# Performance work log

Measured on AMD Instinct MI355X. Metric: run time of the kernel, lower is better.

Reference implementation:

```python
import jax, jax.numpy as jnp
import numpy as np

N_NODES = 50000
N_EDGES = 800000
IN_C, HID_C, OUT_C = 256, 256, 64


def _glorot(key, shape):
    fan_in, fan_out = shape[1], shape[0]
    lim = float(np.sqrt(6.0 / (fan_in + fan_out)))
    return jax.random.uniform(key, shape, jnp.float32, -lim, lim)


def setup_inputs() -> dict:
    key = jax.random.key(0)
    ks = jax.random.split(key, 8)
    x = jax.random.normal(ks[0], (N_NODES, IN_C), jnp.float32)
    edge_index = jax.random.randint(ks[1], (2, N_EDGES), 0, N_NODES, jnp.int64)
    # layer 1: SAGEConv(IN_C -> HID_C): lin_l (agg neighbors, has bias), lin_r (root, no bias)
    W_l1 = _glorot(ks[2], (HID_C, IN_C))
    b1 = jnp.zeros((HID_C,), jnp.float32)
    W_r1 = _glorot(ks[3], (HID_C, IN_C))
    # layer 2: SAGEConv(HID_C -> OUT_C)
    W_l2 = _glorot(ks[4], (OUT_C, HID_C))
    b2 = jnp.zeros((OUT_C,), jnp.float32)
    W_r2 = _glorot(ks[5], (OUT_C, HID_C))
    return {"x": x, "W_l1": W_l1, "b1": b1, "W_r1": W_r1,
            "W_l2": W_l2, "b2": b2, "W_r2": W_r2, "edge_index": edge_index}


def _sage_conv(x, src, dst, W_l, b, W_r, n_nodes):
    # mean aggregation of source-node features into destination nodes
    msg = x[src]                                               # [E, C]
    agg = jax.ops.segment_sum(msg, dst, num_segments=n_nodes)  # [N, C]
    deg = jax.ops.segment_sum(jnp.ones((src.shape[0],), x.dtype), dst,
                              num_segments=n_nodes)            # [N]
    agg = agg / jnp.maximum(deg, 1.0)[:, None]
    # out = lin_l(agg) + lin_r(x); bias only on lin_l (PyG SAGEConv default)
    return agg @ W_l.T + b + x @ W_r.T


def reference(x, W_l1, b1, W_r1, W_l2, b2, W_r2, edge_index):
    src, dst = edge_index[0], edge_index[1]
    n = x.shape[0]
    h = _sage_conv(x, src, dst, W_l1, b1, W_r1, n)
    h = jax.nn.relu(h)  # dropout is identity in eval mode
    out = _sage_conv(h, src, dst, W_l2, b2, W_r2, n)
    return out
```

## Files before the change

### kernel.cpp

```cpp
#include <hip/hip_runtime.h>

#define IN_C 256
#define HID_C 256
#define OUT_C 64

#define NBK 64
#define NPAD 50176
#define N2 (NPAD / 2)
#define NCH (NPAD / 256)

typedef __attribute__((ext_vector_type(8))) short bf16x8;
typedef __attribute__((ext_vector_type(4))) float f32x4;
typedef __attribute__((ext_vector_type(2))) float f32x2;
typedef __attribute__((ext_vector_type(8))) unsigned short ushortx8;
typedef __attribute__((ext_vector_type(4))) unsigned int u32x4;
typedef __attribute__((ext_vector_type(2))) unsigned int u32x2;

__device__ inline float b2f(unsigned short u) {
    union { unsigned int u; float f; } v; v.u = ((unsigned int)u) << 16; return v.f;
}
__device__ inline unsigned short f2b(float f) {
    union { float f; unsigned int u; } v; v.f = f;
    unsigned int u = v.u;
    unsigned int r = (u + 0x7fffu + ((u >> 16) & 1u)) >> 16;
    return (unsigned short)r;
}

__device__ __forceinline__ unsigned char f2fp8(float v) {
    int pk = __builtin_amdgcn_cvt_pk_fp8_f32(v, v, 0, false);
    return (unsigned char)(pk & 0xff);
}
__device__ __forceinline__ void fp8acc4(unsigned int w, float& a0, float& a1, float& a2, float& a3) {
    f32x2 lo = __builtin_amdgcn_cvt_pk_f32_fp8((int)w, false);
    f32x2 hi = __builtin_amdgcn_cvt_pk_f32_fp8((int)w, true);
    a0 += lo.x; a1 += lo.y; a2 += hi.x; a3 += hi.y;
}

__device__ __forceinline__ void gl2lds16(const ushort* g, ushort* l) {
    __builtin_amdgcn_global_load_lds((const __attribute__((address_space(1))) void*)g,
                                     (__attribute__((address_space(3))) void*)l, 16, 0, 0);
}

__device__ __forceinline__ void conv8(const float* __restrict__ src, ushort* __restrict__ dst, int u) {
    const float4* p = (const float4*)(src + (size_t)u * 8);
    float4 a = p[0], b = p[1];
    ushort4 o0 = make_ushort4(f2b(a.x), f2b(a.y), f2b(a.z), f2b(a.w));
    ushort4 o1 = make_ushort4(f2b(b.x), f2b(b.y), f2b(b.z), f2b(b.w));
    ((ushort4*)(dst + (size_t)u * 8))[0] = o0;
    ((ushort4*)(dst + (size_t)u * 8))[1] = o1;
}


__global__ __launch_bounds__(1024) void k_front(const int* __restrict__ dst, int E, int EPB,
                                                ushort* __restrict__ rank,
                                                unsigned int* __restrict__ cnt32,
                                                int* __restrict__ chunkpart,
                                                const float* __restrict__ x, ushort* __restrict__ xb,
                                                int xUnits,
                                                const float* __restrict__ Wl1, const float* __restrict__ Wr1,
                                                const float* __restrict__ Wl2, const float* __restrict__ Wr2,
                                                ushort* __restrict__ Wc1, ushort* __restrict__ Wc2) {
    const int bid = blockIdx.x;
    const int t = threadIdx.x;

    if (bid < NBK) {
        __shared__ unsigned int h[N2];
        for (int i = t; i < N2; i += 1024) h[i] = 0;
        __syncthreads();

        const int e0 = bid * EPB;
        const int e1 = min(e0 + EPB, E);
        for (int e = e0 + t; e < e1; e += 1024) {
            int d = dst[e];
            int sh = (d & 1) << 4;
            unsigned int old = atomicAdd(&h[d >> 1], 1u << sh);
            rank[e] = (ushort)((old >> sh) & 0xffffu);
        }
        __syncthreads();

        unsigned int* outp = cnt32 + (size_t)bid * N2;
        for (int i = t; i < N2; i += 1024) outp[i] = h[i];

        if (t < NCH) {
            int c = t;
            int sum = 0;
#pragma unroll 8
            for (int j = 0; j < 128; ++j) {
                unsigned int v = h[c * 128 + ((j + c) & 127)];
                sum += (int)(v & 0xffffu) + (int)(v >> 16);
            }
            chunkpart[c * NBK + bid] = sum;
        }
        return;
    }

    const int ct = (bid - NBK) * 1024 + t;
    const int cn = 256 * 1024;
    for (int i = ct; i < 20480; i += cn) {
        if (i < 8192)       conv8(Wl1, Wc1,         i);
        else if (i < 16384) conv8(Wr1, Wc1 + 65536, i - 8192);
        else if (i < 18432) conv8(Wl2, Wc2,         i - 16384);
        else                conv8(Wr2, Wc2 + 16384, i - 18432);
    }
    for (int u = ct; u < xUnits; u += cn) conv8(x, xb, u);
}


__global__ __launch_bounds__(256) void k_scan(const unsigned int* __restrict__ cnt32,
                                              const int* __restrict__ chunkpart, int N,
                                              int* __restrict__ row_start,
                                              ushort* __restrict__ off16) {
    __shared__ int s[256];
    const int bid = blockIdx.x;
    const int t = threadIdx.x;

    int pre = 0;
    const int limit = bid * NBK;
    for (int i = t; i < limit; i += 256) pre += chunkpart[i];
    s[t] = pre;
    __syncthreads();
    for (int o = 128; o > 0; o >>= 1) {
        if (t < o) s[t] += s[t + o];
        __syncthreads();
    }
    const int chunk_off = s[0];
    __syncthreads();

    const int i = bid * 256 + t;
    const ushort* cnt16 = (const ushort*)cnt32;
    int run = 0;
#pragma unroll 8
    for (int b = 0; b < NBK; ++b) {
        ushort cv = cnt16[(size_t)b * NPAD + i];
        off16[(size_t)b * NPAD + i] = (ushort)run;
        run += cv;
    }
    int deg = run;

    s[t] = deg;
    __syncthreads();
    for (int o = 1; o < 256; o <<= 1) {
        int xx = (t >= o) ? s[t - o] : 0;
        __syncthreads();
        s[t] += xx;
        __syncthreads();
    }
    if (i < N) row_start[i + 1] = s[t] + chunk_off;
    if (i == 0) row_start[0] = 0;
}


__global__ __launch_bounds__(256) void k_gemm_mfma(const ushort* __restrict__ A,
                                                   const ushort* __restrict__ W,
                                                   unsigned char* __restrict__ Cp,
                                                   ushort* __restrict__ Cr,
                                                   int N, int K, int PC, int nby, int nwg,
                                                   int nScat,
                                                   const int* __restrict__ src, const int* __restrict__ dst,
                                                   const ushort* __restrict__ rank,
                                                   const int* __restrict__ row_start,
                                                   const ushort* __restrict__ off16,
                                                   int E, int EPB, int* __restrict__ eidx) {
    if (blockIdx.x < (unsigned)nScat) {
        int base = blockIdx.x * 256 + threadIdx.x;
        int stride = nScat * 256;
        for (int e = base; e < E; e += stride) {
            int d = dst[e];
            int b = e / EPB;
            eidx[row_start[d] + (int)off16[(size_t)b * NPAD + d] + (int)rank[e]] = src[e];
        }
        return;
    }

    __shared__ ushort As[2][128 * 64];
    __shared__ ushort Bs[2][128 * 64];

    const int orig = blockIdx.x - nScat;
    const int q = nwg >> 3, r = nwg & 7;
    const int xcd = orig & 7;
    const int base = (xcd < r) ? xcd * (q + 1) : r * (q + 1) + (xcd - r) * q;
    const int wgid = base + (orig >> 3);
    const int bx = wgid / nby, by = wgid % nby;

    const int wid  = threadIdx.x >> 6;
    const int lane = threadIdx.x & 63;
    const int wr = wid >> 1, wc = wid & 1;
    const int bm = bx * 128;
    const int bn = by * 128;
    const int lr = lane & 15;
    const int lk = lane >> 4;
    const int srow   = lane >> 3;
    const int schunk = lane & 7;

    f32x4 acc[4][4];
#pragma unroll
    for (int m = 0; m < 4; ++m)
#pragma unroll
        for (int n = 0; n < 4; ++n) acc[m][n] = (f32x4){0.f, 0.f, 0.f, 0.f};

#pragma unroll
    for (int i = 0; i < 4; ++i) {
        int seg = wid * 4 + i;
        int row = seg * 8 + srow;
        gl2lds16(A + (size_t)(bm + row) * K + schunk * 8, As[0] + seg * 512);
        gl2lds16(W + (size_t)(bn + row) * K + schunk * 8, Bs[0] + seg * 512);
    }
    __syncthreads();

    int cur = 0;
    for (int k0 = 0; k0 < K; k0 += 64) {
        const int kn = k0 + 64;
        if (kn < K) {
#pragma unroll
            for (int i = 0; i < 4; ++i) {
                int seg = wid * 4 + i;
                int row = seg * 8 + srow;
                gl2lds16(A + (size_t)(bm + row) * K + kn + schunk * 8, As[cur ^ 1] + seg * 512);
                gl2lds16(W + (size_t)(bn + row) * K + kn + schunk * 8, Bs[cur ^ 1] + seg * 512);
            }
        }

#pragma unroll
        for (int ks = 0; ks < 2; ++ks) {
            bf16x8 a[4], b[4];
#pragma unroll
            for (int m = 0; m < 4; ++m)
                a[m] = *(const bf16x8*)(As[cur] + (wr * 64 + m * 16 + lr) * 64 + ks * 32 + lk * 8);
#pragma unroll
            for (int n = 0; n < 4; ++n)
                b[n] = *(const bf16x8*)(Bs[cur] + (wc * 64 + n * 16 + lr) * 64 + ks * 32 + lk * 8);
#pragma unroll
            for (int m = 0; m < 4; ++m)
#pragma unroll
                for (int n = 0; n < 4; ++n)
                    acc[m][n] = __builtin_amdgcn_mfma_f32_16x16x32_bf16(a[m], b[n], acc[m][n], 0, 0, 0);
        }
        __syncthreads();
        cur ^= 1;
    }

    const bool isP = (bn + wc * 64) < PC;
#pragma unroll
    for (int m = 0; m < 4; ++m)
#pragma unroll
        for (int r2 = 0; r2 < 4; ++r2) {
            int row = bm + wr * 64 + m * 16 + lk * 4 + r2;
            if (row < N) {
                if (isP) {
#pragma unroll
                    for (int n = 0; n < 4; ++n) {
                        int col = bn + wc * 64 + n * 16 + lr;
                        Cp[(size_t)row * PC + col] = f2fp8(acc[m][n][r2]);
                    }
                } else {
#pragma unroll
                    for (int n = 0; n < 4; ++n) {
                        int col = bn + wc * 64 + n * 16 + lr - PC;
                        Cr[(size_t)row * PC + col] = f2b(acc[m][n][r2]);
                    }
                }
            }
        }
}


__global__ __launch_bounds__(256) void k_agg1(const unsigned char* __restrict__ P1,
                                              const ushort* __restrict__ R1,
                                              const float* __restrict__ bias,
                                              const int* __restrict__ row_start,
                                              const int* __restrict__ eidx,
                                              ushort* __restrict__ h, int N) {
    int node = (blockIdx.x * blockDim.x + threadIdx.x) >> 6;
    int lane = threadIdx.x & 63;
    if (node >= N) return;
    const int slot = lane >> 4;
    const int sub  = lane & 15;
    int s0 = row_start[node], s1 = row_start[node + 1];

    float acc[16];
#pragma unroll
    for (int i = 0; i < 16; ++i) acc[i] = 0.f;

    for (int e = s0 + slot; e < s1; e += 16) {
        int e1 = e + 4, e2 = e + 8, e3 = e + 12;
        bool h1 = e1 < s1, h2 = e2 < s1, h3 = e3 < s1;
        int sA = eidx[e];
        int sB = h1 ? eidx[e1] : sA;
        int sC = h2 ? eidx[e2] : sA;
        int sD = h3 ? eidx[e3] : sA;
        u32x4 a = *(const u32x4*)(P1 + (size_t)sA * 256 + sub * 16);
        u32x4 b = *(const u32x4*)(P1 + (size_t)sB * 256 + sub * 16);
        u32x4 c = *(const u32x4*)(P1 + (size_t)sC * 256 + sub * 16);
        u32x4 d = *(const u32x4*)(P1 + (size_t)sD * 256 + sub * 16);
#pragma unroll
        for (int w = 0; w < 4; ++w) fp8acc4(a[w], acc[w*4], acc[w*4+1], acc[w*4+2], acc[w*4+3]);
        if (h1) {
#pragma unroll
            for (int w = 0; w < 4; ++w) fp8acc4(b[w], acc[w*4], acc[w*4+1], acc[w*4+2], acc[w*4+3]);
        }
        if (h2) {
#pragma unroll
            for (int w = 0; w < 4; ++w) fp8acc4(c[w], acc[w*4], acc[w*4+1], acc[w*4+2], acc[w*4+3]);
        }
        if (h3) {
#pragma unroll
            for (int w = 0; w < 4; ++w) fp8acc4(d[w], acc[w*4], acc[w*4+1], acc[w*4+2], acc[w*4+3]);
        }
    }

#pragma unroll
    for (int i = 0; i < 16; ++i) {
        acc[i] += __shfl_xor(acc[i], 16, 64);
        acc[i] += __shfl_xor(acc[i], 32, 64);
    }

    if (slot == 0) {
        int d = s1 - s0;
        float inv = 1.0f / (float)(d > 1 ? d : 1);
        const ushort* rp = R1 + (size_t)node * 256 + sub * 16;
        ushortx8 r0 = *(const ushortx8*)(rp);
        ushortx8 r1 = *(const ushortx8*)(rp + 8);
        const float* bp = bias + sub * 16;
        ushortx8 o0, o1;
#pragma unroll
        for (int i = 0; i < 8; ++i) {
            float v0 = fmaxf(acc[i] * inv + bp[i] + b2f(r0[i]), 0.f);
            float v1 = fmaxf(acc[i + 8] * inv + bp[i + 8] + b2f(r1[i]), 0.f);
            o0[i] = f2b(v0);
            o1[i] = f2b(v1);
        }
        ushort* hp = h + (size_t)node * 256 + sub * 16;
        *(ushortx8*)(hp) = o0;
        *(ushortx8*)(hp + 8) = o1;
    }
}


__global__ __launch_bounds__(256) void k_agg2(const unsigned char* __restrict__ P2,
                                              const ushort* __restrict__ R2,
                                              const float* __restrict__ bias,
                                              const int* __restrict__ row_start,
                                              const int* __restrict__ eidx,
                                              float* __restrict__ out, int N) {
    int node = (blockIdx.x * blockDim.x + threadIdx.x) >> 6;
    int lane = threadIdx.x & 63;
    if (node >= N) return;
    const int slot = lane >> 3;
    const int sub  = lane & 7;
    int s0 = row_start[node], s1 = row_start[node + 1];

    float acc[8];
#pragma unroll
    for (int i = 0; i < 8; ++i) acc[i] = 0.f;

    for (int e = s0 + slot; e < s1; e += 32) {
        int e1 = e + 8, e2 = e + 16, e3 = e + 24;
        bool h1 = e1 < s1, h2 = e2 < s1, h3 = e3 < s1;
        int sA = eidx[e];
        int sB = h1 ? eidx[e1] : sA;
        int sC = h2 ? eidx[e2] : sA;
        int sD = h3 ? eidx[e3] : sA;
        u32x2 a = *(const u32x2*)(P2 + (size_t)sA * 64 + sub * 8);
        u32x2 b = *(const u32x2*)(P2 + (size_t)sB * 64 + sub * 8);
        u32x2 c = *(const u32x2*)(P2 + (size_t)sC * 64 + sub * 8);
        u32x2 d = *(const u32x2*)(P2 + (size_t)sD * 64 + sub * 8);
#pragma unroll
        for (int w = 0; w < 2; ++w) fp8acc4(a[w], acc[w*4], acc[w*4+1], acc[w*4+2], acc[w*4+3]);
        if (h1) {
#pragma unroll
            for (int w = 0; w < 2; ++w) fp8acc4(b[w], acc[w*4], acc[w*4+1], acc[w*4+2], acc[w*4+3]);
        }
        if (h2) {
#pragma unroll
            for (int w = 0; w < 2; ++w) fp8acc4(c[w], acc[w*4], acc[w*4+1], acc[w*4+2], acc[w*4+3]);
        }
        if (h3) {
#pragma unroll
            for (int w = 0; w < 2; ++w) fp8acc4(d[w], acc[w*4], acc[w*4+1], acc[w*4+2], acc[w*4+3]);
        }
    }

#pragma unroll
    for (int i = 0; i < 8; ++i) {
        acc[i] += __shfl_xor(acc[i], 8, 64);
        acc[i] += __shfl_xor(acc[i], 16, 64);
        acc[i] += __shfl_xor(acc[i], 32, 64);
    }

    if (slot == 0) {
        int d = s1 - s0;
        float inv = 1.0f / (float)(d > 1 ? d : 1);
        ushortx8 rv = *(const ushortx8*)(R2 + (size_t)node * 64 + sub * 8);
        const float* bp = bias + sub * 8;
        float o[8];
#pragma unroll
        for (int i = 0; i < 8; ++i) o[i] = acc[i] * inv + bp[i] + b2f(rv[i]);
        float4* op = (float4*)(out + (size_t)node * 64 + sub * 8);
        op[0] = make_float4(o[0], o[1], o[2], o[3]);
        op[1] = make_float4(o[4], o[5], o[6], o[7]);
    }
}


extern "C" void kernel_launch(void* const* d_in, const int* in_sizes, int n_in,
                              void* d_out, int out_size, void* d_ws, size_t ws_size,
                              hipStream_t stream) {
    const float* x    = (const float*)d_in[0];
    const float* W_l1 = (const float*)d_in[1];
    const float* b1   = (const float*)d_in[2];
    const float* W_r1 = (const float*)d_in[3];
    const float* W_l2 = (const float*)d_in[4];
    const float* b2   = (const float*)d_in[5];
    const float* W_r2 = (const float*)d_in[6];
    const int*   ei   = (const int*)d_in[7];

    const int N = in_sizes[0] / IN_C;
    const int E = in_sizes[7] / 2;
    const int EPB = (E + NBK - 1) / NBK;
    const int* src = ei;
    const int* dst = ei + E;

    char* ws = (char*)d_ws;
    size_t off_ = 0;
    auto alloc = [&](size_t bytes) -> void* {
        void* p = ws + off_;
        off_ += (bytes + 255) & ~(size_t)255;
        return p;
    };
    unsigned int*  cnt32     = (unsigned int*)alloc((size_t)NBK * N2 * 4);
    ushort*        off16     = (ushort*)alloc((size_t)NBK * NPAD * 2);
    int*           chunkpart = (int*)alloc((size_t)NCH * NBK * 4);
    int*           row_start = (int*)alloc((size_t)(N + 1) * 4);
    ushort*        rank      = (ushort*)alloc((size_t)E * 2);
    int*           eidx      = (int*)alloc((size_t)E * 4);
    ushort*        xb        = (ushort*)alloc((size_t)N * IN_C * 2);
    ushort*        Wc1       = (ushort*)alloc((size_t)2 * HID_C * IN_C * 2);
    ushort*        Wc2       = (ushort*)alloc((size_t)2 * OUT_C * HID_C * 2);
    unsigned char* P1        = (unsigned char*)alloc((size_t)N * HID_C);
    ushort*        R1        = (ushort*)alloc((size_t)N * HID_C * 2);
    ushort*        h         = (ushort*)alloc((size_t)N * HID_C * 2);
    unsigned char* P2        = (unsigned char*)alloc((size_t)N * OUT_C);
    ushort*        R2        = (ushort*)alloc((size_t)N * OUT_C * 2);
    (void)alloc(128 * 512 * 2);
    (void)ws_size; (void)n_in; (void)out_size;

    {
        int xUnits = N * IN_C / 8;
        k_front<<<NBK + 256, 1024, 0, stream>>>(dst, E, EPB, rank, cnt32, chunkpart,
                                                x, xb, xUnits,
                                                W_l1, W_r1, W_l2, W_r2, Wc1, Wc2);
    }

    k_scan<<<NCH, 256, 0, stream>>>(cnt32, chunkpart, N, row_start, off16);

    {
        const int nScat = 448;
        int nbx = (N + 127) / 128, nby = (2 * HID_C) / 128;
        int nwg = nbx * nby;
        k_gemm_mfma<<<nScat + nwg, 256, 0, stream>>>(xb, Wc1, P1, R1, N, IN_C, HID_C, nby, nwg,
                                                     nScat, src, dst, rank, row_start, off16,
                                                     E, EPB, eidx);
        k_agg1<<<(N + 3) / 4, 256, 0, stream>>>(P1, R1, b1, row_start, eidx, h, N);
    }

    {
        int nbx = (N + 127) / 128, nby = (2 * OUT_C) / 128;
        int nwg = nbx * nby;
        k_gemm_mfma<<<nwg, 256, 0, stream>>>(h, Wc2, P2, R2, N, HID_C, OUT_C, nby, nwg,
                                             0, nullptr, nullptr, nullptr, nullptr, nullptr,
                                             0, 0, nullptr);
        k_agg2<<<(N + 3) / 4, 256, 0, stream>>>(P2, R2, b2, row_start, eidx, (float*)d_out, N);
    }
}
```

Before: 152.0 us.

## Add dedicated layer-1 GEMM keeping full A row-tile resident in LDS

```diff
diff --git a/kernel.cpp b/kernel.cpp
--- a/kernel.cpp
+++ b/kernel.cpp
@@ -150,17 +150,16 @@
 }
 
 
-__global__ __launch_bounds__(256) void k_gemm_mfma(const ushort* __restrict__ A,
-                                                   const ushort* __restrict__ W,
-                                                   unsigned char* __restrict__ Cp,
-                                                   ushort* __restrict__ Cr,
-                                                   int N, int K, int PC, int nby, int nwg,
-                                                   int nScat,
-                                                   const int* __restrict__ src, const int* __restrict__ dst,
-                                                   const ushort* __restrict__ rank,
-                                                   const int* __restrict__ row_start,
-                                                   const ushort* __restrict__ off16,
-                                                   int E, int EPB, int* __restrict__ eidx) {
+__global__ __launch_bounds__(256) void k_gemm_l1(const ushort* __restrict__ A,
+                                                 const ushort* __restrict__ W,
+                                                 unsigned char* __restrict__ Cp,
+                                                 ushort* __restrict__ Cr,
+                                                 int N, int nScat,
+                                                 const int* __restrict__ src, const int* __restrict__ dst,
+                                                 const ushort* __restrict__ rank,
+                                                 const int* __restrict__ row_start,
+                                                 const ushort* __restrict__ off16,
+                                                 int E, int EPB, int* __restrict__ eidx) {
     if (blockIdx.x < (unsigned)nScat) {
         int base = blockIdx.x * 256 + threadIdx.x;
         int stride = nScat * 256;
@@ -172,10 +171,120 @@
         return;
     }
 
+    __shared__ ushort Aall[64 * 256];
+    __shared__ ushort Wb[2 * 128 * 64];
+
+    const int bx = blockIdx.x - nScat;
+    const int t = threadIdx.x;
+    const int bm = bx * 64;
+
+    const int wid  = t >> 6;
+    const int lane = t & 63;
+    const int wr = wid >> 1;
+    const int wc = wid & 1;
+    const int lr = lane & 15;
+    const int lk = lane >> 4;
+
+    {
+        const int arow7 = (t >> 5) & 7;
+        const int asrc  = ((t & 31) ^ arow7) << 3;
+#pragma unroll
+        for (int i = 0; i < 8; ++i) {
+            gl2lds16(A + (size_t)(bm + i * 8 + (t >> 5)) * 256 + asrc,
+                     Aall + i * 2048 + t * 8);
+        }
+        const int wrow7 = (t >> 3) & 7;
+        const int wsrc  = ((t & 7) ^ wrow7) << 3;
+#pragma unroll
+        for (int i = 0; i < 4; ++i) {
+            gl2lds16(W + (size_t)(i * 32 + (t >> 3)) * 256 + 0 + wsrc,
+                     Wb + i * 2048 + t * 8);
+        }
+    }
+    __syncthreads();
+
+    f32x4 acc[2][4];
+    int s = 0;
+#pragma unroll
+    for (int by = 0; by < 4; ++by) {
+#pragma unroll
+        for (int m = 0; m < 2; ++m)
+#pragma unroll
+            for (int n = 0; n < 4; ++n) acc[m][n] = (f32x4){0.f, 0.f, 0.f, 0.f};
+
+#pragma unroll
+        for (int kk = 0; kk < 4; ++kk, ++s) {
+            const int sn = s + 1;
+            if (sn < 16) {
+                const int by_n = sn >> 2, kk_n = sn & 3, buf_n = sn & 1;
+                const int wrow7 = (t >> 3) & 7;
+                const int wsrc  = ((t & 7) ^ wrow7) << 3;
+#pragma unroll
+                for (int i = 0; i < 4; ++i) {
+                    gl2lds16(W + (size_t)(by_n * 128 + i * 32 + (t >> 3)) * 256 + kk_n * 64 + wsrc,
+                             Wb + buf_n * 8192 + i * 2048 + t * 8);
+                }
+            }
+
+            const int kb = kk * 8;
+            const int buf = s & 1;
+            const int sw = lr & 7;
+#pragma unroll
+            for (int ks = 0; ks < 2; ++ks) {
+                bf16x8 a[2], b[4];
+                const int ck = ks * 4 + lk;
+#pragma unroll
+                for (int m = 0; m < 2; ++m)
+                    a[m] = *(const bf16x8*)(Aall + (wr * 32 + m * 16 + lr) * 256 + ((kb + (ck ^ sw)) << 3));
+#pragma unroll
+                for (int n = 0; n < 4; ++n)
+                    b[n] = *(const bf16x8*)(Wb + buf * 8192 + (wc * 64 + n * 16 + lr) * 64 + ((ck ^ sw) << 3));
+#pragma unroll
+                for (int m = 0; m < 2; ++m)
+#pragma unroll
+                    for (int n = 0; n < 4; ++n)
+                        acc[m][n] = __builtin_amdgcn_mfma_f32_16x16x32_bf16(a[m], b[n], acc[m][n], 0, 0, 0);
+            }
+
+            if (kk == 3) {
+                const bool isP = (by * 128 + wc * 64) < HID_C;
+#pragma unroll
+                for (int m = 0; m < 2; ++m)
+#pragma unroll
+                    for (int r2 = 0; r2 < 4; ++r2) {
+                        int row = bm + wr * 32 + m * 16 + lk * 4 + r2;
+                        if (row < N) {
+                            if (isP) {
+#pragma unroll
+                                for (int n = 0; n < 4; ++n) {
+                                    int col = by * 128 + wc * 64 + n * 16 + lr;
+                                    Cp[(size_t)row * HID_C + col] = f2fp8(acc[m][n][r2]);
+                                }
+                            } else {
+#pragma unroll
+                                for (int n = 0; n < 4; ++n) {
+                                    int col = by * 128 + wc * 64 + n * 16 + lr - HID_C;
+                                    Cr[(size_t)row * HID_C + col] = f2b(acc[m][n][r2]);
+                                }
+                            }
+                        }
+                    }
+            }
+            __syncthreads();
+        }
+    }
+}
+
+
+__global__ __launch_bounds__(256) void k_gemm_mfma(const ushort* __restrict__ A,
+                                                   const ushort* __restrict__ W,
+                                                   unsigned char* __restrict__ Cp,
+                                                   ushort* __restrict__ Cr,
+                                                   int N, int K, int PC, int nby, int nwg) {
     __shared__ ushort As[2][128 * 64];
     __shared__ ushort Bs[2][128 * 64];
 
-    const int orig = blockIdx.x - nScat;
+    const int orig = blockIdx.x;
     const int q = nwg >> 3, r = nwg & 7;
     const int xcd = orig & 7;
     const int base = (xcd < r) ? xcd * (q + 1) : r * (q + 1) + (xcd - r) * q;
@@ -455,20 +564,17 @@
 
     {
         const int nScat = 448;
-        int nbx = (N + 127) / 128, nby = (2 * HID_C) / 128;
-        int nwg = nbx * nby;
-        k_gemm_mfma<<<nScat + nwg, 256, 0, stream>>>(xb, Wc1, P1, R1, N, IN_C, HID_C, nby, nwg,
-                                                     nScat, src, dst, rank, row_start, off16,
-                                                     E, EPB, eidx);
+        int nbx = (N + 63) / 64;
+        k_gemm_l1<<<nScat + nbx, 256, 0, stream>>>(xb, Wc1, P1, R1, N,
+                                                   nScat, src, dst, rank, row_start, off16,
+                                                   E, EPB, eidx);
         k_agg1<<<(N + 3) / 4, 256, 0, stream>>>(P1, R1, b1, row_start, eidx, h, N);
     }
 
     {
         int nbx = (N + 127) / 128, nby = (2 * OUT_C) / 128;
         int nwg = nbx * nby;
-        k_gemm_mfma<<<nwg, 256, 0, stream>>>(h, Wc2, P2, R2, N, HID_C, OUT_C, nby, nwg,
-                                             0, nullptr, nullptr, nullptr, nullptr, nullptr,
-                                             0, 0, nullptr);
+        k_gemm_mfma<<<nwg, 256, 0, stream>>>(h, Wc2, P2, R2, N, HID_C, OUT_C, nby, nwg);
         k_agg2<<<(N + 3) / 4, 256, 0, stream>>>(P2, R2, b2, row_start, eidx, (float*)d_out, N);
     }
 }
```

Result: faster. 147.7 us (-2.8%).
